# Optimization experiments

Measured on AMD Instinct MI355X. Metric: run time of the kernel, lower is better.

The kernel has to match this reference:

```python
import jax, jax.numpy as jnp
import numpy as np

T, B, F = 197, 64, 768      # tokens (hardcoded 197 in module), batch, width
N, K = 8, 2                 # num_experts, top-k
CAP = int(197 * 1.0 * K / N)  # capacity = 49
H = 4 * F                   # expert hidden (c_fc out)
G = F // 4                  # gate hidden


def setup_inputs() -> dict:
    key = jax.random.key(0)
    ks = jax.random.split(key, 9)
    s = 0.02
    return {
        "x":   jax.random.normal(ks[0], (T, B, F), jnp.float32),
        # gate: Linear(F, F/4) -> ReLU -> Linear(F/4, N)
        "Wg1": jax.random.normal(ks[1], (F, G), jnp.float32) * s,
        "bg1": jnp.zeros((G,), jnp.float32),
        "Wg2": jax.random.normal(ks[2], (G, N), jnp.float32) * s,
        "bg2": jnp.zeros((N,), jnp.float32),
        # experts: per-expert Linear(F, 4F) -> ReLU -> Linear(4F, F), stacked over N
        "W1":  jax.random.normal(ks[3], (N, F, H), jnp.float32) * s,
        "b1":  jnp.zeros((N, H), jnp.float32),
        "W2":  jax.random.normal(ks[4], (N, H, F), jnp.float32) * s,
        "b2":  jnp.zeros((N, F), jnp.float32),
    }


def reference(x, Wg1, bg1, Wg2, bg2, W1, b1, W2, b2):
    # gating: softmax over experts (dim=2)
    logits = jax.nn.relu(x @ Wg1 + bg1) @ Wg2 + bg2          # [T,B,N]
    gw = jax.nn.softmax(logits, axis=2)                      # [T,B,N]

    # dense all-expert MLP (as-written: every expert on every token)
    h = jax.nn.relu(jnp.einsum('tbf,nfh->tbnh', x, W1) + b1)  # [T,B,N,H]
    eo = jnp.einsum('tbnh,nhf->tbnf', h, W2) + b2             # [T,B,N,F]

    # top-k expert mask (dim=2)
    _, idx = jax.lax.top_k(gw, K)                             # [T,B,K]
    mask_exp = jnp.any(jnp.arange(N)[None, None, None, :] == idx[..., None], axis=2)
    cw = gw * mask_exp                                        # [T,B,N]

    # capacity mask: top-CAP tokens per (batch, expert) along dim 0
    cwT = jnp.moveaxis(cw, 0, -1)                             # [B,N,T]
    _, idx2 = jax.lax.top_k(cwT, CAP)                         # [B,N,CAP]
    mask_cap = jnp.any(jnp.arange(T)[None, None, None, :] == idx2[..., None], axis=2)  # [B,N,T]
    fw = cw * jnp.moveaxis(mask_cap, -1, 0)                   # [T,B,N]

    # combine selected expert outputs, residual-style subtract
    out = jnp.einsum('tbnf,tbn->tbf', eo, fw) - x             # [T,B,F]
    return out
```

## Files before the change

### kernel.cpp

```cpp
#include <hip/hip_runtime.h>
#include <hip/hip_bf16.h>
#include <math.h>
#include <stdint.h>

#define T_ 197
#define B_ 64
#define F_ 768
#define N_ 8
#define CAP_ 49
#define H_ 3072
#define G_ 192
#define TB_ (T_*B_)
#define NBN_ (B_*N_)
#define ME_ 3200
#define MR_ 3136
#define MT_ 25600
#define KH_ 4
#define HP_ 768
#define NBLK_ 1200
#define HCF_ 384
#define NPF_ 8

using bf16x8 = __attribute__((ext_vector_type(8))) short;
using f32x4  = __attribute__((ext_vector_type(4))) float;

__device__ __forceinline__ unsigned short f2bf(float v) {
    __hip_bfloat16 h = __float2bfloat16(v);
    return __builtin_bit_cast(unsigned short, h);
}
__device__ __forceinline__ float bf2f(unsigned short u) {
    unsigned int w = ((unsigned int)u) << 16;
    return __builtin_bit_cast(float, w);
}
__device__ __forceinline__ unsigned int add2bf(unsigned int a, unsigned int b) {
    float al = bf2f((unsigned short)(a & 0xffff)), ah = bf2f((unsigned short)(a >> 16));
    float bl = bf2f((unsigned short)(b & 0xffff)), bh = bf2f((unsigned short)(b >> 16));
    return (unsigned int)f2bf(al + bl) | ((unsigned int)f2bf(ah + bh) << 16);
}

#define GLL16(g, l) __builtin_amdgcn_global_load_lds( \
    (const __attribute__((address_space(1))) unsigned int*)(uintptr_t)(g), \
    (__attribute__((address_space(3))) unsigned int*)(uintptr_t)(l), 16, 0, 0)

__device__ __forceinline__ int xcd_swz(int bid, int nblk) {
    int q = nblk >> 3, r = nblk & 7;
    int xcd = bid & 7, idx = bid >> 3;
    int base = (xcd < r) ? xcd * (q + 1) : r * (q + 1) + (xcd - r) * q;
    return base + idx;
}

__global__ void k_init_out(const float* __restrict__ x, float* __restrict__ out) {
    int i = blockIdx.x * blockDim.x + threadIdx.x;
    const float4* xv = (const float4*)x;
    float4* ov = (float4*)out;
    float4 v = xv[i];
    ov[i] = make_float4(-v.x, -v.y, -v.z, -v.w);
}

__global__ __launch_bounds__(256) void k_gate1(
        const float* __restrict__ x, const float* __restrict__ Wg1,
        float* __restrict__ gs_part) {
    __shared__ float xs[32][68];
    __shared__ float wt[32][200];
    int bm = blockIdx.x % 197, kh = blockIdx.x / 197;
    int m0 = bm * 64, k0 = kh * (F_ / KH_);
    int tid = threadIdx.x, lane = tid & 63, wid = tid >> 6;
    int mg = lane & 15;
    int ng = (lane >> 4) + 4 * wid;
    f32x4 acc[4][3] = {};

    int xr = tid >> 3, xc = tid & 7;
    float4 xreg0, xreg1;
    float4 wreg[6];

    auto loadRegs = [&](int t) {
        int kb = k0 + t * 32;
        xreg0 = *(const float4*)(x + (size_t)(m0 + xr) * F_ + kb + xc * 4);
        xreg1 = *(const float4*)(x + (size_t)(m0 + xr + 32) * F_ + kb + xc * 4);
        #pragma unroll
        for (int i = 0; i < 6; ++i) {
            int idx = tid + i * 256;
            int kr = idx / 48, nc = idx % 48;
            wreg[i] = *(const float4*)(Wg1 + (size_t)(kb + kr) * G_ + nc * 4);
        }
    };
    auto writeLDS = [&]() {
        xs[xc * 4 + 0][xr] = xreg0.x;  xs[xc * 4 + 1][xr] = xreg0.y;
        xs[xc * 4 + 2][xr] = xreg0.z;  xs[xc * 4 + 3][xr] = xreg0.w;
        xs[xc * 4 + 0][xr + 32] = xreg1.x;  xs[xc * 4 + 1][xr + 32] = xreg1.y;
        xs[xc * 4 + 2][xr + 32] = xreg1.z;  xs[xc * 4 + 3][xr + 32] = xreg1.w;
        #pragma unroll
        for (int i = 0; i < 6; ++i) {
            int idx = tid + i * 256;
            int kr = idx / 48, nc = idx % 48;
            *(float4*)&wt[kr][nc * 4] = wreg[i];
        }
    };

    loadRegs(0);
    for (int t = 0; t < 6; ++t) {
        __syncthreads();
        writeLDS();
        __syncthreads();
        if (t < 5) loadRegs(t + 1);
        #pragma unroll
        for (int k = 0; k < 32; ++k) {
            float4 av = *(const float4*)&xs[k][mg * 4];
            float4 b0 = *(const float4*)&wt[k][ng * 12];
            float4 b1 = *(const float4*)&wt[k][ng * 12 + 4];
            float4 b2 = *(const float4*)&wt[k][ng * 12 + 8];
            float am[4] = {av.x, av.y, av.z, av.w};
            #pragma unroll
            for (int mi = 0; mi < 4; ++mi) {
                acc[mi][0][0] += am[mi] * b0.x; acc[mi][0][1] += am[mi] * b0.y;
                acc[mi][0][2] += am[mi] * b0.z; acc[mi][0][3] += am[mi] * b0.w;
                acc[mi][1][0] += am[mi] * b1.x; acc[mi][1][1] += am[mi] * b1.y;
                acc[mi][1][2] += am[mi] * b1.z; acc[mi][1][3] += am[mi] * b1.w;
                acc[mi][2][0] += am[mi] * b2.x; acc[mi][2][1] += am[mi] * b2.y;
                acc[mi][2][2] += am[mi] * b2.z; acc[mi][2][3] += am[mi] * b2.w;
            }
        }
    }
    float* gp = gs_part + (size_t)kh * TB_ * G_;
    #pragma unroll
    for (int mi = 0; mi < 4; ++mi) {
        int r = m0 + mg * 4 + mi;
        #pragma unroll
        for (int jv = 0; jv < 3; ++jv)
            *(f32x4*)(gp + (size_t)r * G_ + ng * 12 + jv * 4) = acc[mi][jv];
    }
}

__global__ __launch_bounds__(256) void k_gate2(
        const float* __restrict__ gs_part, const float* __restrict__ bg1,
        const float* __restrict__ Wg2, const float* __restrict__ bg2,
        float* __restrict__ cw, int* __restrict__ ecnt) {
    __shared__ float gsh[32][200];
    __shared__ float wg2s[G_ * N_];
    __shared__ float lg[32][8];
    int tid = threadIdx.x;
    int id0 = blockIdx.x * 32;

    for (int i = tid; i < 32 * 48; i += 256) {
        int r = i / 48, c4 = i % 48;
        const float* p0 = gs_part + (size_t)(id0 + r) * G_ + c4 * 4;
        float4 a = *(const float4*)p0;
        float4 b = *(const float4*)(p0 + (size_t)TB_ * G_);
        float4 c = *(const float4*)(p0 + 2 * (size_t)TB_ * G_);
        float4 d = *(const float4*)(p0 + 3 * (size_t)TB_ * G_);
        float4 g = *(const float4*)(bg1 + c4 * 4);
        float4 v;
        v.x = fmaxf(a.x + b.x + c.x + d.x + g.x, 0.f);
        v.y = fmaxf(a.y + b.y + c.y + d.y + g.y, 0.f);
        v.z = fmaxf(a.z + b.z + c.z + d.z + g.z, 0.f);
        v.w = fmaxf(a.w + b.w + c.w + d.w + g.w, 0.f);
        ((float4*)&gsh[r][0])[c4] = v;
    }
    for (int i = tid; i < G_ * N_; i += 256) wg2s[i] = Wg2[i];
    __syncthreads();

    int tk = tid >> 3, n = tid & 7;
    float a = bg2[n];
    for (int k = 0; k < G_; ++k) a += gsh[tk][k] * wg2s[k * N_ + n];
    lg[tk][n] = a;
    __syncthreads();

    if (tid < 32) {
        int tk2 = tid;
        float p[8];
        float m = lg[tk2][0];
        #pragma unroll
        for (int nn = 1; nn < 8; ++nn) m = fmaxf(m, lg[tk2][nn]);
        float s = 0.f;
        #pragma unroll
        for (int nn = 0; nn < 8; ++nn) { p[nn] = expf(lg[tk2][nn] - m); s += p[nn]; }
        float inv = 1.f / s;
        #pragma unroll
        for (int nn = 0; nn < 8; ++nn) p[nn] *= inv;
        int i1 = 0; float v1 = p[0];
        #pragma unroll
        for (int nn = 1; nn < 8; ++nn) if (p[nn] > v1) { v1 = p[nn]; i1 = nn; }
        int i2 = -1; float v2 = -1.f;
        #pragma unroll
        for (int nn = 0; nn < 8; ++nn) if (nn != i1 && p[nn] > v2) { v2 = p[nn]; i2 = nn; }
        int id = id0 + tk2;
        int t = id / B_, b = id % B_;
        ecnt[id] = 0;
        #pragma unroll
        for (int nn = 0; nn < 8; ++nn) {
            float v = (nn == i1 || nn == i2) ? p[nn] : 0.f;
            cw[((size_t)(b * N_ + nn)) * T_ + t] = v;
        }
    }
}

__global__ __launch_bounds__(256) void k_gate(
        const float* __restrict__ x, const float* __restrict__ Wg1,
        const float* __restrict__ bg1, const float* __restrict__ Wg2,
        const float* __restrict__ bg2, float* __restrict__ cw,
        int* __restrict__ ecnt) {
    __shared__ float xsh[8][F_];
    __shared__ float gsl[8][G_];
    __shared__ float lg[8][N_];
    int tid = threadIdx.x;
    int id0 = blockIdx.x * 8;

    int gid = blockIdx.x * 256 + tid;
    if (gid < TB_ && ecnt) ecnt[gid] = 0;

    const float4* xv = (const float4*)(x + (size_t)id0 * F_);
    float4* xshv = (float4*)&xsh[0][0];
    for (int idx = tid; idx < 8 * (F_/4); idx += 256) xshv[idx] = xv[idx];
    __syncthreads();

    if (tid < G_) {
        float acc[8];
        float bb = bg1[tid];
        #pragma unroll
        for (int tk = 0; tk < 8; ++tk) acc[tk] = bb;
        for (int k = 0; k < F_; ++k) {
            float w = Wg1[k * G_ + tid];
            #pragma unroll
            for (int tk = 0; tk < 8; ++tk) acc[tk] += xsh[tk][k] * w;
        }
        #pragma unroll
        for (int tk = 0; tk < 8; ++tk) gsl[tk][tid] = fmaxf(acc[tk], 0.f);
    }
    __syncthreads();

    if (tid < 64) {
        int tk = tid >> 3, n = tid & 7;
        float acc = bg2[n];
        for (int k = 0; k < G_; ++k) acc += gsl[tk][k] * Wg2[k * N_ + n];
        lg[tk][n] = acc;
    }
    __syncthreads();

    if (tid < 8) {
        int tk = tid;
        float p[8];
        float m = lg[tk][0];
        #pragma unroll
        for (int n = 1; n < 8; ++n) m = fmaxf(m, lg[tk][n]);
        float s = 0.f;
        #pragma unroll
        for (int n = 0; n < 8; ++n) { p[n] = expf(lg[tk][n] - m); s += p[n]; }
        float inv = 1.f / s;
        #pragma unroll
        for (int n = 0; n < 8; ++n) p[n] *= inv;
        int i1 = 0; float v1 = p[0];
        #pragma unroll
        for (int n = 1; n < 8; ++n) if (p[n] > v1) { v1 = p[n]; i1 = n; }
        int i2 = -1; float v2 = -1.f;
        #pragma unroll
        for (int n = 0; n < 8; ++n) if (n != i1 && p[n] > v2) { v2 = p[n]; i2 = n; }
        int id = id0 + tk;
        int t = id / B_, b = id % B_;
        #pragma unroll
        for (int n = 0; n < 8; ++n) {
            float v = (n == i1 || n == i2) ? p[n] : 0.f;
            cw[((size_t)(b * N_ + n)) * T_ + t] = v;
        }
    }
}

__global__ __launch_bounds__(256) void k_capacity(
        const float* __restrict__ cw, int* __restrict__ toks,
        float* __restrict__ wts, int* __restrict__ counts,
        int* __restrict__ ecnt, int* __restrict__ erow) {
    __shared__ float v[T_];
    __shared__ int keep[T_];
    int tid = threadIdx.x;
    int bn = blockIdx.x;
    int b = bn >> 3, n = bn & 7;
    if (tid < T_) v[tid] = cw[(size_t)bn * T_ + tid];
    __syncthreads();
    int kp = 0; float my = 0.f;
    if (tid < T_) {
        my = v[tid];
        int rank = 0;
        for (int t2 = 0; t2 < T_; ++t2) {
            float vt = v[t2];
            rank += (vt > my) || (vt == my && t2 < tid);
        }
        kp = (rank < CAP_) && (my > 0.f);
    }
    if (tid < T_) keep[tid] = kp;
    __syncthreads();
    if (tid < T_ && kp) {
        int slot = 0;
        for (int t2 = 0; t2 < T_; ++t2) slot += (t2 < tid) ? keep[t2] : 0;
        toks[bn * CAP_ + slot] = tid;
        wts[bn * CAP_ + slot] = my;
        if (ecnt) {
            int orow = tid * B_ + b;
            int pos = atomicAdd(&ecnt[orow], 1);
            erow[orow * 2 + pos] = n * ME_ + b * CAP_ + slot;
        }
    }
    if (tid == 0) {
        int tot = 0;
        for (int t2 = 0; t2 < T_; ++t2) tot += keep[t2];
        counts[bn] = tot;
    }
}

__global__ __launch_bounds__(256) void k_repack(
        const float* __restrict__ W, unsigned short* __restrict__ WT, int K, int J) {
    __shared__ float tile[64][65];
    int bid = blockIdx.x;
    int nk = K >> 6, nj = J >> 6;
    int kt = bid % nk; bid /= nk;
    int jt = bid % nj; int e = bid / nj;
    int k0 = kt * 64, j0 = jt * 64;
    int tid = threadIdx.x;
    int jr = (tid & 15) << 2;
    int kr = tid >> 4;
    const float* src = W + ((size_t)e * K + k0) * J + j0;
    #pragma unroll
    for (int i = 0; i < 4; ++i) {
        float4 v = *(const float4*)(src + (size_t)(kr + 16 * i) * J + jr);
        *(float4*)&tile[kr + 16 * i][jr] = v;
    }
    __syncthreads();
    int c = tid & 7;
    int jrow = tid >> 3;
    #pragma unroll
    for (int i = 0; i < 2; ++i) {
        int j = jrow + 32 * i;
        float f[8];
        #pragma unroll
        for (int s = 0; s < 8; ++s) f[s] = tile[c * 8 + s][j];
        uint4 u;
        u.x = f2bf(f[0]) | ((unsigned)f2bf(f[1]) << 16);
        u.y = f2bf(f[2]) | ((unsigned)f2bf(f[3]) << 16);
        u.z = f2bf(f[4]) | ((unsigned)f2bf(f[5]) << 16);
        u.w = f2bf(f[6]) | ((unsigned)f2bf(f[7]) << 16);
        int jg = j0 + j;
        char* drow = (char*)WT + ((size_t)e * J + jg) * (size_t)K * 2 + (size_t)(k0 >> 6) * 128;
        *(uint4*)(drow + ((c << 4) ^ ((jg & 7) << 4))) = u;
    }
}

__global__ __launch_bounds__(256) void k_gather(
        const float* __restrict__ x, const int* __restrict__ toks,
        const int* __restrict__ counts, unsigned short* __restrict__ Xg) {
    int gi = blockIdx.x * 256 + threadIdx.x;
    int R = gi / 96, c = gi - R * 96;
    int e = R / ME_, re = R - e * ME_;
    uint4 val = make_uint4(0u, 0u, 0u, 0u);
    if (re < MR_) {
        int g = re / CAP_, slot = re - g * CAP_;
        int bn = g * N_ + e;
        if (slot < counts[bn]) {
            int t = toks[bn * CAP_ + slot];
            const float* xp = x + ((size_t)t * B_ + g) * F_ + c * 8;
            float4 v0 = *(const float4*)xp;
            float4 v1 = *(const float4*)(xp + 4);
            val.x = f2bf(v0.x) | ((unsigned)f2bf(v0.y) << 16);
            val.y = f2bf(v0.z) | ((unsigned)f2bf(v0.w) << 16);
            val.z = f2bf(v1.x) | ((unsigned)f2bf(v1.y) << 16);
            val.w = f2bf(v1.z) | ((unsigned)f2bf(v1.w) << 16);
        }
    }
    int w = (c * 16) & 127;
    char* dst = (char*)Xg + (size_t)R * 1536 + (c >> 3) * 128 + (w ^ ((R & 7) << 4));
    *(uint4*)dst = val;
}

__global__ __launch_bounds__(256) void k_gemm1(
        const unsigned short* __restrict__ W1T, const unsigned short* __restrict__ Xg,
        const float* __restrict__ b1, unsigned short* __restrict__ Hg, int pass) {
    __shared__ char ldsA[2][16384];
    __shared__ char ldsB[2][16384];
    int swzb = xcd_swz(blockIdx.x, NBLK_);
    int e = swzb / 150;
    int rem = swzb - e * 150;
    int mt = rem / 6, jt = rem % 6;
    int tid = threadIdx.x, lane = tid & 63, wid = tid >> 6;
    int lr8 = lane >> 3, sl = (lane & 7) << 4;
    const char* Ab = (const char*)W1T + ((size_t)e * H_ + pass * HP_ + jt * 128) * (F_ * 2);
    const char* Bb = (const char*)Xg + ((size_t)e * ME_ + mt * 128) * (F_ * 2);
    f32x4 acc[4][4] = {};
    int swz = (lane & 7) << 4;
    int q16 = (lane >> 4) << 4;

    auto stage = [&](int buf, int it) {
        int kb = it << 7;
        #pragma unroll
        for (int i = 0; i < 4; ++i) {
            int lr = wid * 32 + i * 8 + lr8;
            GLL16(Ab + (size_t)lr * 1536 + kb + sl, ldsA[buf] + (wid * 32 + i * 8) * 128);
            GLL16(Bb + (size_t)lr * 1536 + kb + sl, ldsB[buf] + (wid * 32 + i * 8) * 128);
        }
    };

    stage(0, 0);
    __syncthreads();
    int cur = 0;
    for (int it = 0; it < 12; ++it) {
        if (it < 11) stage(cur ^ 1, it + 1);
        const char* la = ldsA[cur] + ((wid & 1) * 64) * 128;
        const char* lb = ldsB[cur] + ((wid >> 1) * 64) * 128;
        #pragma unroll
        for (int ks = 0; ks < 2; ++ks) {
            bf16x8 af[4], bfr[4];
            int kk = (ks * 64 + q16) ^ swz;
            #pragma unroll
            for (int t = 0; t < 4; ++t) {
                int ro = (16 * t + (lane & 15)) * 128;
                af[t]  = *(const bf16x8*)(la + ro + kk);
                bfr[t] = *(const bf16x8*)(lb + ro + kk);
            }
            #pragma unroll
            for (int ti = 0; ti < 4; ++ti)
                #pragma unroll
                for (int tm = 0; tm < 4; ++tm)
                    acc[ti][tm] = __builtin_amdgcn_mfma_f32_16x16x32_bf16(af[ti], bfr[tm], acc[ti][tm], 0, 0, 0);
        }
        __syncthreads();
        cur ^= 1;
    }
    char* tile = &ldsA[0][0];
    int jl0 = (wid & 1) * 64;
    int ml0 = (wid >> 1) * 64;
    const float* b1p = b1 + (size_t)e * H_ + pass * HP_ + jt * 128;
    #pragma unroll
    for (int tj = 0; tj < 4; ++tj) {
        int jc = jl0 + 16 * tj + ((lane >> 4) << 2);
        float bb0 = b1p[jc], bb1 = b1p[jc + 1], bb2 = b1p[jc + 2], bb3 = b1p[jc + 3];
        #pragma unroll
        for (int tm = 0; tm < 4; ++tm) {
            int m = ml0 + 16 * tm + (lane & 15);
            f32x4 a = acc[tj][tm];
            unsigned int u0 = f2bf(fmaxf(a[0] + bb0, 0.f)) | ((unsigned)f2bf(fmaxf(a[1] + bb1, 0.f)) << 16);
            unsigned int u1 = f2bf(fmaxf(a[2] + bb2, 0.f)) | ((unsigned)f2bf(fmaxf(a[3] + bb3, 0.f)) << 16);
            int bcol = jc * 2;
            int w = bcol & 127;
            *(uint2*)(tile + m * 256 + (bcol & ~127) + (w ^ ((m & 7) << 4))) = make_uint2(u0, u1);
        }
    }
    __syncthreads();
    char* Hrow = (char*)Hg + ((size_t)e * ME_ + mt * 128) * (HP_ * 2) + (size_t)jt * 256;
    #pragma unroll
    for (int i = 0; i < 8; ++i) {
        int idx = tid + i * 256;
        int r = idx >> 4, c = (idx & 15) << 4;
        *(uint4*)(Hrow + (size_t)r * (HP_ * 2) + c) = *(const uint4*)(tile + r * 256 + c);
    }
}

__global__ __launch_bounds__(256) void k_gemm2(
        const unsigned short* __restrict__ W2T, const unsigned short* __restrict__ Hg,
        const float* __restrict__ b2, const float* __restrict__ wts,
        const int* __restrict__ counts, unsigned short* __restrict__ Og, int pass) {
    __shared__ char ldsA[2][16384];
    __shared__ char ldsB[2][16384];
    int swzb = xcd_swz(blockIdx.x, NBLK_);
    int e = swzb / 150;
    int rem = swzb - e * 150;
    int mt = rem / 6, ft = rem % 6;
    int tid = threadIdx.x, lane = tid & 63, wid = tid >> 6;
    int lr8 = lane >> 3, sl = (lane & 7) << 4;
    const char* Ab = (const char*)W2T + ((size_t)e * F_ + ft * 128) * (H_ * 2) + (size_t)pass * (HP_ * 2);
    const char* Bb = (const char*)Hg + ((size_t)e * ME_ + mt * 128) * (HP_ * 2);
    f32x4 acc[4][4] = {};
    int swz = (lane & 7) << 4;
    int q16 = (lane >> 4) << 4;

    auto stage = [&](int buf, int it) {
        int kb = it << 7;
        #pragma unroll
        for (int i = 0; i < 4; ++i) {
            int lr = wid * 32 + i * 8 + lr8;
            GLL16(Ab + (size_t)lr * 6144 + kb + sl, ldsA[buf] + (wid * 32 + i * 8) * 128);
            GLL16(Bb + (size_t)lr * 1536 + kb + sl, ldsB[buf] + (wid * 32 + i * 8) * 128);
        }
    };

    stage(0, 0);
    __syncthreads();
    int cur = 0;
    for (int it = 0; it < 12; ++it) {
        if (it < 11) stage(cur ^ 1, it + 1);
        const char* la = ldsA[cur] + ((wid & 1) * 64) * 128;
        const char* lb = ldsB[cur] + ((wid >> 1) * 64) * 128;
        #pragma unroll
        for (int ks = 0; ks < 2; ++ks) {
            bf16x8 af[4], bfr[4];
            int kk = (ks * 64 + q16) ^ swz;
            #pragma unroll
            for (int t = 0; t < 4; ++t) {
                int ro = (16 * t + (lane & 15)) * 128;
                af[t]  = *(const bf16x8*)(la + ro + kk);
                bfr[t] = *(const bf16x8*)(lb + ro + kk);
            }
            #pragma unroll
            for (int ti = 0; ti < 4; ++ti)
                #pragma unroll
                for (int tm = 0; tm < 4; ++tm)
                    acc[ti][tm] = __builtin_amdgcn_mfma_f32_16x16x32_bf16(af[ti], bfr[tm], acc[ti][tm], 0, 0, 0);
        }
        __syncthreads();
        cur ^= 1;
    }
    char* tile = &ldsA[0][0];
    int fl0 = (wid & 1) * 64;
    int ml0 = (wid >> 1) * 64;
    const float* b2p = b2 + (size_t)e * F_ + (size_t)ft * 128;
    float fwv[4];
    #pragma unroll
    for (int tm = 0; tm < 4; ++tm) {
        int mloc = ml0 + 16 * tm + (lane & 15);
        int re = mt * 128 + mloc;
        float fw = 0.f;
        if (re < MR_) {
            int g = re / CAP_;
            int slot = re - g * CAP_;
            int bn = g * N_ + e;
            if (slot < counts[bn]) fw = wts[bn * CAP_ + slot];
        }
        fwv[tm] = fw;
    }
    #pragma unroll
    for (int tf = 0; tf < 4; ++tf) {
        int fc = fl0 + 16 * tf + ((lane >> 4) << 2);
        float c0 = 0.f, c1 = 0.f, c2 = 0.f, c3 = 0.f;
        if (pass == 0) { c0 = b2p[fc]; c1 = b2p[fc + 1]; c2 = b2p[fc + 2]; c3 = b2p[fc + 3]; }
        #pragma unroll
        for (int tm = 0; tm < 4; ++tm) {
            int mloc = ml0 + 16 * tm + (lane & 15);
            f32x4 a = acc[tf][tm];
            float fw = fwv[tm];
            unsigned int u0 = f2bf(fw * (a[0] + c0)) | ((unsigned)f2bf(fw * (a[1] + c1)) << 16);
            unsigned int u1 = f2bf(fw * (a[2] + c2)) | ((unsigned)f2bf(fw * (a[3] + c3)) << 16);
            int bcol = fc * 2;
            int w = bcol & 127;
            *(uint2*)(tile + mloc * 256 + (bcol & ~127) + (w ^ ((mloc & 7) << 4))) = make_uint2(u0, u1);
        }
    }
    __syncthreads();
    char* Orow = (char*)Og + ((size_t)e * ME_ + mt * 128) * (F_ * 2) + (size_t)ft * 256;
    if (pass == 0) {
        #pragma unroll
        for (int i = 0; i < 8; ++i) {
            int idx = tid + i * 256;
            int r = idx >> 4, c = (idx & 15) << 4;
            const char* src = tile + r * 256 + (c & ~127) + ((c & 127) ^ ((r & 7) << 4));
            *(uint4*)(Orow + (size_t)r * (F_ * 2) + c) = *(const uint4*)src;
        }
    } else {
        #pragma unroll
        for (int i = 0; i < 8; ++i) {
            int idx = tid + i * 256;
            int r = idx >> 4, c = (idx & 15) << 4;
            const char* src = tile + r * 256 + (c & ~127) + ((c & 127) ^ ((r & 7) << 4));
            uint4 nw = *(const uint4*)src;
            uint4* dst = (uint4*)(Orow + (size_t)r * (F_ * 2) + c);
            uint4 old = *dst;
            uint4 res;
            res.x = add2bf(old.x, nw.x);
            res.y = add2bf(old.y, nw.y);
            res.z = add2bf(old.z, nw.z);
            res.w = add2bf(old.w, nw.w);
            *dst = res;
        }
    }
}

__global__ __launch_bounds__(256) void k_combine(
        const float* __restrict__ x, const unsigned short* __restrict__ Og,
        const int* __restrict__ ecnt, const int* __restrict__ erow,
        float* __restrict__ out) {
    int idx = blockIdx.x * 256 + threadIdx.x;
    int row = idx / 192, c4 = idx - row * 192;
    float4 s = make_float4(0.f, 0.f, 0.f, 0.f);
    int c = ecnt[row];
    if (c > 0) {
        ushort4 u = *(const ushort4*)(Og + (size_t)erow[row * 2] * F_ + c4 * 4);
        s.x += bf2f(u.x); s.y += bf2f(u.y); s.z += bf2f(u.z); s.w += bf2f(u.w);
    }
    if (c > 1) {
        ushort4 u = *(const ushort4*)(Og + (size_t)erow[row * 2 + 1] * F_ + c4 * 4);
        s.x += bf2f(u.x); s.y += bf2f(u.y); s.z += bf2f(u.z); s.w += bf2f(u.w);
    }
    float4 xv = ((const float4*)x)[idx];
    ((float4*)out)[idx] = make_float4(s.x - xv.x, s.y - xv.y, s.z - xv.z, s.w - xv.w);
}

__global__ __launch_bounds__(HCF_) void k_fc1(
        const float* __restrict__ x, const float* __restrict__ W1,
        const float* __restrict__ b1, const int* __restrict__ toks,
        const int* __restrict__ counts, __hip_bfloat16* __restrict__ h, int pass) {
    __shared__ float xs[25][F_];
    int tid = threadIdx.x;
    int bn = blockIdx.x >> 1;
    int half = blockIdx.x & 1;
    int r0 = half * 25;
    int b = bn >> 3, n = bn & 7;
    int c = counts[bn];
    for (int idx = tid; idx < 25 * (F_/4); idx += HCF_) {
        int r = idx / (F_/4), k4 = idx % (F_/4);
        int gr = r0 + r;
        float4 val = make_float4(0.f, 0.f, 0.f, 0.f);
        if (gr < c) {
            int t = toks[bn * CAP_ + gr];
            val = ((const float4*)(x + ((size_t)(t * B_ + b)) * F_))[k4];
        }
        ((float4*)&xs[r][0])[k4] = val;
    }
    __syncthreads();
    int j = pass * HCF_ + tid;
    const float* w1p = W1 + (size_t)n * F_ * H_ + j;
    float bias = b1[n * H_ + j];
    float acc[25];
    #pragma unroll
    for (int r = 0; r < 25; ++r) acc[r] = bias;
    const float4* xsv = (const float4*)&xs[0][0];
    for (int k4 = 0; k4 < F_/4; ++k4) {
        float w0 = w1p[(size_t)(4*k4+0) * H_];
        float w1v = w1p[(size_t)(4*k4+1) * H_];
        float w2v = w1p[(size_t)(4*k4+2) * H_];
        float w3v = w1p[(size_t)(4*k4+3) * H_];
        #pragma unroll
        for (int r = 0; r < 25; ++r) {
            float4 xv = xsv[r * (F_/4) + k4];
            acc[r] += xv.x*w0 + xv.y*w1v + xv.z*w2v + xv.w*w3v;
        }
    }
    __hip_bfloat16* hp = h + ((size_t)bn * CAP_ + r0) * HCF_ + tid;
    #pragma unroll
    for (int r = 0; r < 25; ++r) {
        int gr = r0 + r;
        if (gr < CAP_) hp[(size_t)r * HCF_] = __float2bfloat16(fmaxf(acc[r], 0.f));
    }
}

__global__ __launch_bounds__(768) void k_fc2(
        const float* __restrict__ W2, const float* __restrict__ b2,
        const int* __restrict__ toks, const float* __restrict__ wts,
        const int* __restrict__ counts, const __hip_bfloat16* __restrict__ h,
        float* __restrict__ out, int pass) {
    __shared__ float hs[CAP_][HCF_];
    int tid = threadIdx.x;
    int bn = blockIdx.x;
    int c = counts[bn];
    if (c == 0) return;
    int b = bn >> 3, n = bn & 7;
    const ushort4* hv = (const ushort4*)(h + (size_t)bn * CAP_ * HCF_);
    for (int idx = tid; idx < CAP_ * (HCF_/4); idx += 768) {
        ushort4 u = hv[idx];
        float4 fv;
        fv.x = __bfloat162float(*(const __hip_bfloat16*)&u.x);
        fv.y = __bfloat162float(*(const __hip_bfloat16*)&u.y);
        fv.z = __bfloat162float(*(const __hip_bfloat16*)&u.z);
        fv.w = __bfloat162float(*(const __hip_bfloat16*)&u.w);
        ((float4*)&hs[0][0])[idx] = fv;
    }
    __syncthreads();
    int f = tid;
    const float* w2p = W2 + (size_t)n * H_ * F_ + (size_t)(pass * HCF_) * F_ + f;
    float acc[CAP_];
    #pragma unroll
    for (int r = 0; r < CAP_; ++r) acc[r] = 0.f;
    for (int j4 = 0; j4 < HCF_/4; ++j4) {
        float w0 = w2p[(size_t)(4*j4+0) * F_];
        float w1v = w2p[(size_t)(4*j4+1) * F_];
        float w2v = w2p[(size_t)(4*j4+2) * F_];
        float w3v = w2p[(size_t)(4*j4+3) * F_];
        #pragma unroll
        for (int r = 0; r < CAP_; ++r) {
            float4 hh = ((const float4*)&hs[r][0])[j4];
            acc[r] += hh.x*w0 + hh.y*w1v + hh.z*w2v + hh.w*w3v;
        }
    }
    float bias = (pass == 0) ? b2[n * F_ + f] : 0.f;
    #pragma unroll
    for (int r = 0; r < CAP_; ++r) {
        if (r < c) {
            int t = toks[bn * CAP_ + r];
            float fw = wts[bn * CAP_ + r];
            atomicAdd(&out[((size_t)(t * B_ + b)) * F_ + f], fw * (acc[r] + bias));
        }
    }
}

extern "C" void kernel_launch(void* const* d_in, const int* in_sizes, int n_in,
                              void* d_out, int out_size, void* d_ws, size_t ws_size,
                              hipStream_t stream) {
    const float* x   = (const float*)d_in[0];
    const float* Wg1 = (const float*)d_in[1];
    const float* bg1 = (const float*)d_in[2];
    const float* Wg2 = (const float*)d_in[3];
    const float* bg2 = (const float*)d_in[4];
    const float* W1  = (const float*)d_in[5];
    const float* b1  = (const float*)d_in[6];
    const float* W2  = (const float*)d_in[7];
    const float* b2  = (const float*)d_in[8];
    float* out = (float*)d_out;

    size_t oW1T  = 0;
    size_t oW2T  = oW1T + (size_t)N_ * H_ * F_ * 2;
    size_t oXg   = oW2T + (size_t)N_ * H_ * F_ * 2;
    size_t oCw   = oXg  + (size_t)MT_ * F_ * 2;
    size_t oWts  = oCw  + (size_t)NBN_ * T_ * 4;
    size_t oTok  = oWts + (size_t)NBN_ * CAP_ * 4;
    size_t oCnt  = oTok + (size_t)NBN_ * CAP_ * 4;
    size_t oEcnt = oCnt + (size_t)NBN_ * 4;
    size_t oErow = oEcnt + (size_t)TB_ * 4;
    size_t oOg   = oErow + (size_t)TB_ * 8;
    size_t oHg   = oOg  + (size_t)MT_ * F_ * 2;
    size_t need  = oHg + (size_t)MT_ * HP_ * 2;

    if (ws_size >= need) {
        unsigned short* W1T = (unsigned short*)((char*)d_ws + oW1T);
        unsigned short* W2T = (unsigned short*)((char*)d_ws + oW2T);
        unsigned short* Xg  = (unsigned short*)((char*)d_ws + oXg);
        unsigned short* Og  = (unsigned short*)((char*)d_ws + oOg);
        unsigned short* Hg  = (unsigned short*)((char*)d_ws + oHg);
        float* gs_part = (float*)((char*)d_ws + oHg);
        float* cw   = (float*)((char*)d_ws + oCw);
        float* wts  = (float*)((char*)d_ws + oWts);
        int* toks   = (int*)((char*)d_ws + oTok);
        int* counts = (int*)((char*)d_ws + oCnt);
        int* ecnt   = (int*)((char*)d_ws + oEcnt);
        int* erow   = (int*)((char*)d_ws + oErow);

        k_gate1<<<197 * KH_, 256, 0, stream>>>(x, Wg1, gs_part);
        k_gate2<<<TB_ / 32, 256, 0, stream>>>(gs_part, bg1, Wg2, bg2, cw, ecnt);
        k_capacity<<<NBN_, 256, 0, stream>>>(cw, toks, wts, counts, ecnt, erow);
        k_repack<<<N_ * (F_/64) * (H_/64), 256, 0, stream>>>(W1, W1T, F_, H_);
        k_repack<<<N_ * (H_/64) * (F_/64), 256, 0, stream>>>(W2, W2T, H_, F_);
        k_gather<<<(MT_ * 96) / 256, 256, 0, stream>>>(x, toks, counts, Xg);
        for (int p = 0; p < 4; ++p) {
            k_gemm1<<<NBLK_, 256, 0, stream>>>(W1T, Xg, b1, Hg, p);
            k_gemm2<<<NBLK_, 256, 0, stream>>>(W2T, Hg, b2, wts, counts, Og, p);
        }
        k_combine<<<(TB_ * 192) / 256, 256, 0, stream>>>(x, Og, ecnt, erow, out);
    } else {
        __hip_bfloat16* h = (__hip_bfloat16*)d_ws;
        float* cw  = (float*)((char*)d_ws + (size_t)NBN_ * CAP_ * HCF_ * 2);
        float* wts = cw + (size_t)NBN_ * T_;
        int* toks  = (int*)(wts + NBN_ * CAP_);
        int* counts = toks + NBN_ * CAP_;
        k_init_out<<<(TB_ * F_) / 1024, 256, 0, stream>>>(x, out);
        k_gate<<<TB_ / 8, 256, 0, stream>>>(x, Wg1, bg1, Wg2, bg2, cw, nullptr);
        k_capacity<<<NBN_, 256, 0, stream>>>(cw, toks, wts, counts, nullptr, nullptr);
        for (int p = 0; p < NPF_; ++p) {
            k_fc1<<<NBN_ * 2, HCF_, 0, stream>>>(x, W1, b1, toks, counts, h, p);
            k_fc2<<<NBN_, 768, 0, stream>>>(W2, b2, toks, wts, counts, h, out, p);
        }
    }
}
```

Measured before the change: 507.0 us.

## Run expert GEMMs unsplit when workspace allows and retile gate GEMM

When the workspace can hold the full hidden activation, the expert MLP runs as one gemm1 launch over all hidden tiles and one gemm2 launch over the full K dimension. This replaces four passes of paired launches and removes the bf16 read-modify-write accumulation of Og between passes. The gate GEMM now uses 128-row tiles with an 8-way K split, and gate2 sums a variable number of partials. The gate partials move to the Og region, and the old four-pass path stays as a fallback when the workspace is smaller.

```diff
diff --git a/kernel.cpp b/kernel.cpp
--- a/kernel.cpp
+++ b/kernel.cpp
@@ -15,9 +15,9 @@
 #define ME_ 3200
 #define MR_ 3136
 #define MT_ 25600
-#define KH_ 4
+#define KH_ 8
+#define GM_ 99
 #define HP_ 768
-#define NBLK_ 1200
 #define HCF_ 384
 #define NPF_ 8
 
@@ -60,23 +60,25 @@
 __global__ __launch_bounds__(256) void k_gate1(
         const float* __restrict__ x, const float* __restrict__ Wg1,
         float* __restrict__ gs_part) {
-    __shared__ float xs[32][68];
-    __shared__ float wt[32][200];
-    int bm = blockIdx.x % 197, kh = blockIdx.x / 197;
-    int m0 = bm * 64, k0 = kh * (F_ / KH_);
-    int tid = threadIdx.x, lane = tid & 63, wid = tid >> 6;
-    int mg = lane & 15;
-    int ng = (lane >> 4) + 4 * wid;
-    f32x4 acc[4][3] = {};
-
-    int xr = tid >> 3, xc = tid & 7;
-    float4 xreg0, xreg1;
+    __shared__ float xs[32][132];
+    __shared__ float wt[32][196];
+    int bm = blockIdx.x % GM_, kh = blockIdx.x / GM_;
+    int m0 = bm * 128, k0 = kh * (F_ / KH_);
+    int tid = threadIdx.x;
+    int mg = tid >> 4;
+    int nq = tid & 15;
+    f32x4 acc[8][3] = {};
+
+    int xm = tid >> 1, xh = tid & 1;
+    int gm = m0 + xm; if (gm >= TB_) gm = TB_ - 1;
+    float4 xreg[4];
     float4 wreg[6];
 
     auto loadRegs = [&](int t) {
         int kb = k0 + t * 32;
-        xreg0 = *(const float4*)(x + (size_t)(m0 + xr) * F_ + kb + xc * 4);
-        xreg1 = *(const float4*)(x + (size_t)(m0 + xr + 32) * F_ + kb + xc * 4);
+        #pragma unroll
+        for (int j = 0; j < 4; ++j)
+            xreg[j] = *(const float4*)(x + (size_t)gm * F_ + kb + (xh * 4 + j) * 4);
         #pragma unroll
         for (int i = 0; i < 6; ++i) {
             int idx = tid + i * 256;
@@ -85,10 +87,14 @@
         }
     };
     auto writeLDS = [&]() {
-        xs[xc * 4 + 0][xr] = xreg0.x;  xs[xc * 4 + 1][xr] = xreg0.y;
-        xs[xc * 4 + 2][xr] = xreg0.z;  xs[xc * 4 + 3][xr] = xreg0.w;
-        xs[xc * 4 + 0][xr + 32] = xreg1.x;  xs[xc * 4 + 1][xr + 32] = xreg1.y;
-        xs[xc * 4 + 2][xr + 32] = xreg1.z;  xs[xc * 4 + 3][xr + 32] = xreg1.w;
+        #pragma unroll
+        for (int j = 0; j < 4; ++j) {
+            int k = (xh * 4 + j) * 4;
+            xs[k + 0][xm] = xreg[j].x;
+            xs[k + 1][xm] = xreg[j].y;
+            xs[k + 2][xm] = xreg[j].z;
+            xs[k + 3][xm] = xreg[j].w;
+        }
         #pragma unroll
         for (int i = 0; i < 6; ++i) {
             int idx = tid + i * 256;
@@ -98,36 +104,37 @@
     };
 
     loadRegs(0);
-    for (int t = 0; t < 6; ++t) {
+    for (int t = 0; t < 3; ++t) {
         __syncthreads();
         writeLDS();
         __syncthreads();
-        if (t < 5) loadRegs(t + 1);
-        #pragma unroll
+        if (t < 2) loadRegs(t + 1);
+        #pragma unroll 4
         for (int k = 0; k < 32; ++k) {
-            float4 av = *(const float4*)&xs[k][mg * 4];
-            float4 b0 = *(const float4*)&wt[k][ng * 12];
-            float4 b1 = *(const float4*)&wt[k][ng * 12 + 4];
-            float4 b2 = *(const float4*)&wt[k][ng * 12 + 8];
-            float am[4] = {av.x, av.y, av.z, av.w};
+            float4 a0 = *(const float4*)&xs[k][mg * 8];
+            float4 a1 = *(const float4*)&xs[k][mg * 8 + 4];
+            f32x4 b0 = *(const f32x4*)&wt[k][nq * 12];
+            f32x4 b1 = *(const f32x4*)&wt[k][nq * 12 + 4];
+            f32x4 b2 = *(const f32x4*)&wt[k][nq * 12 + 8];
+            float am[8] = {a0.x, a0.y, a0.z, a0.w, a1.x, a1.y, a1.z, a1.w};
             #pragma unroll
-            for (int mi = 0; mi < 4; ++mi) {
-                acc[mi][0][0] += am[mi] * b0.x; acc[mi][0][1] += am[mi] * b0.y;
-                acc[mi][0][2] += am[mi] * b0.z; acc[mi][0][3] += am[mi] * b0.w;
-                acc[mi][1][0] += am[mi] * b1.x; acc[mi][1][1] += am[mi] * b1.y;
-                acc[mi][1][2] += am[mi] * b1.z; acc[mi][1][3] += am[mi] * b1.w;
-                acc[mi][2][0] += am[mi] * b2.x; acc[mi][2][1] += am[mi] * b2.y;
-                acc[mi][2][2] += am[mi] * b2.z; acc[mi][2][3] += am[mi] * b2.w;
+            for (int mi = 0; mi < 8; ++mi) {
+                acc[mi][0] += b0 * am[mi];
+                acc[mi][1] += b1 * am[mi];
+                acc[mi][2] += b2 * am[mi];
             }
         }
     }
     float* gp = gs_part + (size_t)kh * TB_ * G_;
     #pragma unroll
-    for (int mi = 0; mi < 4; ++mi) {
-        int r = m0 + mg * 4 + mi;
-        #pragma unroll
-        for (int jv = 0; jv < 3; ++jv)
-            *(f32x4*)(gp + (size_t)r * G_ + ng * 12 + jv * 4) = acc[mi][jv];
+    for (int mi = 0; mi < 8; ++mi) {
+        int r = m0 + mg * 8 + mi;
+        if (r < TB_) {
+            float* rp = gp + (size_t)r * G_ + nq * 12;
+            *(f32x4*)(rp + 0) = acc[mi][0];
+            *(f32x4*)(rp + 4) = acc[mi][1];
+            *(f32x4*)(rp + 8) = acc[mi][2];
+        }
     }
 }
 
@@ -144,16 +151,15 @@
     for (int i = tid; i < 32 * 48; i += 256) {
         int r = i / 48, c4 = i % 48;
         const float* p0 = gs_part + (size_t)(id0 + r) * G_ + c4 * 4;
-        float4 a = *(const float4*)p0;
-        float4 b = *(const float4*)(p0 + (size_t)TB_ * G_);
-        float4 c = *(const float4*)(p0 + 2 * (size_t)TB_ * G_);
-        float4 d = *(const float4*)(p0 + 3 * (size_t)TB_ * G_);
         float4 g = *(const float4*)(bg1 + c4 * 4);
-        float4 v;
-        v.x = fmaxf(a.x + b.x + c.x + d.x + g.x, 0.f);
-        v.y = fmaxf(a.y + b.y + c.y + d.y + g.y, 0.f);
-        v.z = fmaxf(a.z + b.z + c.z + d.z + g.z, 0.f);
-        v.w = fmaxf(a.w + b.w + c.w + d.w + g.w, 0.f);
+        float4 v = g;
+        #pragma unroll
+        for (int p = 0; p < KH_; ++p) {
+            float4 a = *(const float4*)(p0 + (size_t)p * TB_ * G_);
+            v.x += a.x; v.y += a.y; v.z += a.z; v.w += a.w;
+        }
+        v.x = fmaxf(v.x, 0.f); v.y = fmaxf(v.y, 0.f);
+        v.z = fmaxf(v.z, 0.f); v.w = fmaxf(v.w, 0.f);
         ((float4*)&gsh[r][0])[c4] = v;
     }
     for (int i = tid; i < G_ * N_; i += 256) wg2s[i] = Wg2[i];
@@ -370,17 +376,20 @@
 
 __global__ __launch_bounds__(256) void k_gemm1(
         const unsigned short* __restrict__ W1T, const unsigned short* __restrict__ Xg,
-        const float* __restrict__ b1, unsigned short* __restrict__ Hg, int pass) {
+        const float* __restrict__ b1, unsigned short* __restrict__ Hg,
+        int njt, int jofs, int hstrideB, int nblk) {
     __shared__ char ldsA[2][16384];
     __shared__ char ldsB[2][16384];
-    int swzb = xcd_swz(blockIdx.x, NBLK_);
-    int e = swzb / 150;
-    int rem = swzb - e * 150;
-    int mt = rem / 6, jt = rem % 6;
+    int swzb = xcd_swz(blockIdx.x, nblk);
+    int per_e = 25 * njt;
+    int e = swzb / per_e;
+    int rem = swzb - e * per_e;
+    int mt = rem / njt, jtl = rem % njt;
+    int jt = jofs + jtl;
     int tid = threadIdx.x, lane = tid & 63, wid = tid >> 6;
     int lr8 = lane >> 3, sl = (lane & 7) << 4;
-    const char* Ab = (const char*)W1T + ((size_t)e * H_ + pass * HP_ + jt * 128) * (F_ * 2);
-    const char* Bb = (const char*)Xg + ((size_t)e * ME_ + mt * 128) * (F_ * 2);
+    const char* Ab = (const char*)W1T + ((size_t)e * H_ + (size_t)jt * 128) * (F_ * 2);
+    const char* Bb = (const char*)Xg + ((size_t)e * ME_ + (size_t)mt * 128) * (F_ * 2);
     f32x4 acc[4][4] = {};
     int swz = (lane & 7) << 4;
     int q16 = (lane >> 4) << 4;
@@ -424,7 +433,7 @@
     char* tile = &ldsA[0][0];
     int jl0 = (wid & 1) * 64;
     int ml0 = (wid >> 1) * 64;
-    const float* b1p = b1 + (size_t)e * H_ + pass * HP_ + jt * 128;
+    const float* b1p = b1 + (size_t)e * H_ + (size_t)jt * 128;
     #pragma unroll
     for (int tj = 0; tj < 4; ++tj) {
         int jc = jl0 + 16 * tj + ((lane >> 4) << 2);
@@ -441,29 +450,30 @@
         }
     }
     __syncthreads();
-    char* Hrow = (char*)Hg + ((size_t)e * ME_ + mt * 128) * (HP_ * 2) + (size_t)jt * 256;
+    char* Hrow = (char*)Hg + ((size_t)e * ME_ + (size_t)mt * 128) * hstrideB + (size_t)jtl * 256;
     #pragma unroll
     for (int i = 0; i < 8; ++i) {
         int idx = tid + i * 256;
         int r = idx >> 4, c = (idx & 15) << 4;
-        *(uint4*)(Hrow + (size_t)r * (HP_ * 2) + c) = *(const uint4*)(tile + r * 256 + c);
+        *(uint4*)(Hrow + (size_t)r * hstrideB + c) = *(const uint4*)(tile + r * 256 + c);
     }
 }
 
 __global__ __launch_bounds__(256) void k_gemm2(
         const unsigned short* __restrict__ W2T, const unsigned short* __restrict__ Hg,
         const float* __restrict__ b2, const float* __restrict__ wts,
-        const int* __restrict__ counts, unsigned short* __restrict__ Og, int pass) {
+        const int* __restrict__ counts, unsigned short* __restrict__ Og,
+        int kiters, int kofsB, int bstrideB, int nblk) {
     __shared__ char ldsA[2][16384];
     __shared__ char ldsB[2][16384];
-    int swzb = xcd_swz(blockIdx.x, NBLK_);
+    int swzb = xcd_swz(blockIdx.x, nblk);
     int e = swzb / 150;
     int rem = swzb - e * 150;
     int mt = rem / 6, ft = rem % 6;
     int tid = threadIdx.x, lane = tid & 63, wid = tid >> 6;
     int lr8 = lane >> 3, sl = (lane & 7) << 4;
-    const char* Ab = (const char*)W2T + ((size_t)e * F_ + ft * 128) * (H_ * 2) + (size_t)pass * (HP_ * 2);
-    const char* Bb = (const char*)Hg + ((size_t)e * ME_ + mt * 128) * (HP_ * 2);
+    const char* Ab = (const char*)W2T + ((size_t)e * F_ + (size_t)ft * 128) * (H_ * 2) + kofsB;
+    const char* Bb = (const char*)Hg + ((size_t)e * ME_ + (size_t)mt * 128) * bstrideB;
     f32x4 acc[4][4] = {};
     int swz = (lane & 7) << 4;
     int q16 = (lane >> 4) << 4;
@@ -474,15 +484,15 @@
         for (int i = 0; i < 4; ++i) {
             int lr = wid * 32 + i * 8 + lr8;
             GLL16(Ab + (size_t)lr * 6144 + kb + sl, ldsA[buf] + (wid * 32 + i * 8) * 128);
-            GLL16(Bb + (size_t)lr * 1536 + kb + sl, ldsB[buf] + (wid * 32 + i * 8) * 128);
+            GLL16(Bb + (size_t)lr * bstrideB + kb + sl, ldsB[buf] + (wid * 32 + i * 8) * 128);
         }
     };
 
     stage(0, 0);
     __syncthreads();
     int cur = 0;
-    for (int it = 0; it < 12; ++it) {
-        if (it < 11) stage(cur ^ 1, it + 1);
+    for (int it = 0; it < kiters; ++it) {
+        if (it < kiters - 1) stage(cur ^ 1, it + 1);
         const char* la = ldsA[cur] + ((wid & 1) * 64) * 128;
         const char* lb = ldsB[cur] + ((wid >> 1) * 64) * 128;
         #pragma unroll
@@ -522,11 +532,12 @@
         }
         fwv[tm] = fw;
     }
+    int p0 = (kofsB == 0);
     #pragma unroll
     for (int tf = 0; tf < 4; ++tf) {
         int fc = fl0 + 16 * tf + ((lane >> 4) << 2);
         float c0 = 0.f, c1 = 0.f, c2 = 0.f, c3 = 0.f;
-        if (pass == 0) { c0 = b2p[fc]; c1 = b2p[fc + 1]; c2 = b2p[fc + 2]; c3 = b2p[fc + 3]; }
+        if (p0) { c0 = b2p[fc]; c1 = b2p[fc + 1]; c2 = b2p[fc + 2]; c3 = b2p[fc + 3]; }
         #pragma unroll
         for (int tm = 0; tm < 4; ++tm) {
             int mloc = ml0 + 16 * tm + (lane & 15);
@@ -540,8 +551,8 @@
         }
     }
     __syncthreads();
-    char* Orow = (char*)Og + ((size_t)e * ME_ + mt * 128) * (F_ * 2) + (size_t)ft * 256;
-    if (pass == 0) {
+    char* Orow = (char*)Og + ((size_t)e * ME_ + (size_t)mt * 128) * (F_ * 2) + (size_t)ft * 256;
+    if (p0) {
         #pragma unroll
         for (int i = 0; i < 8; ++i) {
             int idx = tid + i * 256;
@@ -710,15 +721,16 @@
     size_t oErow = oEcnt + (size_t)TB_ * 4;
     size_t oOg   = oErow + (size_t)TB_ * 8;
     size_t oHg   = oOg  + (size_t)MT_ * F_ * 2;
-    size_t need  = oHg + (size_t)MT_ * HP_ * 2;
-
-    if (ws_size >= need) {
+    size_t needB = oHg + (size_t)MT_ * HP_ * 2;
+    size_t needA = oHg + (size_t)MT_ * H_ * 2;
+
+    if (ws_size >= needB) {
         unsigned short* W1T = (unsigned short*)((char*)d_ws + oW1T);
         unsigned short* W2T = (unsigned short*)((char*)d_ws + oW2T);
         unsigned short* Xg  = (unsigned short*)((char*)d_ws + oXg);
         unsigned short* Og  = (unsigned short*)((char*)d_ws + oOg);
         unsigned short* Hg  = (unsigned short*)((char*)d_ws + oHg);
-        float* gs_part = (float*)((char*)d_ws + oHg);
+        float* gs_part = (float*)((char*)d_ws + oOg);
         float* cw   = (float*)((char*)d_ws + oCw);
         float* wts  = (float*)((char*)d_ws + oWts);
         int* toks   = (int*)((char*)d_ws + oTok);
@@ -726,15 +738,20 @@
         int* ecnt   = (int*)((char*)d_ws + oEcnt);
         int* erow   = (int*)((char*)d_ws + oErow);
 
-        k_gate1<<<197 * KH_, 256, 0, stream>>>(x, Wg1, gs_part);
+        k_gate1<<<GM_ * KH_, 256, 0, stream>>>(x, Wg1, gs_part);
         k_gate2<<<TB_ / 32, 256, 0, stream>>>(gs_part, bg1, Wg2, bg2, cw, ecnt);
         k_capacity<<<NBN_, 256, 0, stream>>>(cw, toks, wts, counts, ecnt, erow);
         k_repack<<<N_ * (F_/64) * (H_/64), 256, 0, stream>>>(W1, W1T, F_, H_);
         k_repack<<<N_ * (H_/64) * (F_/64), 256, 0, stream>>>(W2, W2T, H_, F_);
         k_gather<<<(MT_ * 96) / 256, 256, 0, stream>>>(x, toks, counts, Xg);
-        for (int p = 0; p < 4; ++p) {
-            k_gemm1<<<NBLK_, 256, 0, stream>>>(W1T, Xg, b1, Hg, p);
-            k_gemm2<<<NBLK_, 256, 0, stream>>>(W2T, Hg, b2, wts, counts, Og, p);
+        if (ws_size >= needA) {
+            k_gemm1<<<4800, 256, 0, stream>>>(W1T, Xg, b1, Hg, 24, 0, H_ * 2, 4800);
+            k_gemm2<<<1200, 256, 0, stream>>>(W2T, Hg, b2, wts, counts, Og, 48, 0, H_ * 2, 1200);
+        } else {
+            for (int p = 0; p < 4; ++p) {
+                k_gemm1<<<1200, 256, 0, stream>>>(W1T, Xg, b1, Hg, 6, p * 6, HP_ * 2, 1200);
+                k_gemm2<<<1200, 256, 0, stream>>>(W2T, Hg, b2, wts, counts, Og, 12, p * HP_ * 2, HP_ * 2, 1200);
+            }
         }
         k_combine<<<(TB_ * 192) / 256, 256, 0, stream>>>(x, Og, ecnt, erow, out);
     } else {
```

Result: slower. 526.9 us (+3.9%).
